# Kernel optimization log

Hardware: AMD Instinct MI355X
Metric: run time of the kernel (lower is better)

The kernel has to match this reference:

```python
import jax, jax.numpy as jnp
import numpy as np

B, T, C, H = 4, 2048, 1024, 16


def setup_inputs() -> dict:
    key = jax.random.key(0)
    k1, k2, k3 = jax.random.split(key, 3)
    x = jax.random.normal(k1, (B, T, C), dtype=jnp.float32)
    W_qkv = jax.random.normal(k2, (C, 3 * C), dtype=jnp.float32) * 0.02
    W_proj = jax.random.normal(k3, (C, C), dtype=jnp.float32) * 0.02
    return {"x": x, "W_qkv": W_qkv, "W_proj": W_proj}


def reference(x, W_qkv, W_proj):
    Bc, Tc, Cc = x.shape
    D = Cc // H
    qkv = x @ W_qkv                          # [B,T,3C]
    k, q, v = jnp.split(qkv, 3, axis=-1)     # split order k,q,v as in source
    q = q.reshape(Bc, Tc, H, D)
    k = k.reshape(Bc, Tc, H, D)
    v = v.reshape(Bc, Tc, H, D)
    # NOTE: module scales by full C**-0.5, not head_dim**-0.5
    scale = jnp.asarray(Cc, x.dtype) ** -0.5
    wei = jnp.einsum("bqhd,bkhd->bhqk", q, k) * scale      # [B,H,T,T]
    causal = jnp.tril(jnp.ones((Tc, Tc), dtype=bool))
    wei = jnp.where(causal[None, None], wei, jnp.asarray(-jnp.inf, x.dtype))
    att = jax.nn.softmax(wei, axis=-1)
    out = jnp.einsum("bhqk,bkhd->bqhd", att, v).reshape(Bc, Tc, Cc)
    return out @ W_proj
```

## Files before the change

kernel.cpp:

```cpp
#include <hip/hip_runtime.h>
#include <hip/hip_bf16.h>

#define B_   4
#define T_   2048
#define C_   1024
#define H_   16
#define D_   64
#define NQKV 3072
#define M_   (B_*T_)

typedef __attribute__((ext_vector_type(8))) short bf16x8;
typedef __attribute__((ext_vector_type(4))) short bf16x4;
typedef __attribute__((ext_vector_type(4))) float f32x4;
typedef __hip_bfloat16 bf16;

__device__ inline short f2bs(float f) {
    bf16 h = __float2bfloat16(f);
    return *(short*)&h;
}

__device__ inline void async_ld16(const bf16* g, const short* l) {
    __builtin_amdgcn_global_load_lds(
        (const __attribute__((address_space(1))) void*)g,
        (__attribute__((address_space(3))) void*)l, 16, 0, 0);
}

__global__ __launch_bounds__(256) void prep(const float* __restrict__ x,
                                            const float* __restrict__ Wqkv,
                                            const float* __restrict__ Wproj,
                                            bf16* __restrict__ xb,
                                            bf16* __restrict__ wqkv_t,
                                            bf16* __restrict__ wproj_t) {
    __shared__ short t[32][33];
    const int bid = blockIdx.x;
    if (bid < 4096) {
        const long i = ((long)bid * 256 + threadIdx.x) * 8;
        const float4 a = *(const float4*)(x + i);
        const float4 bq = *(const float4*)(x + i + 4);
        bf16x8 o;
        o[0] = f2bs(a.x); o[1] = f2bs(a.y); o[2] = f2bs(a.z); o[3] = f2bs(a.w);
        o[4] = f2bs(bq.x); o[5] = f2bs(bq.y); o[6] = f2bs(bq.z); o[7] = f2bs(bq.w);
        *(bf16x8*)(xb + i) = o;
        return;
    }
    const float* in;  bf16* out;  int R, Ccol, r0, c0;
    if (bid < 7168) {
        const int b2 = bid - 4096;
        in = Wqkv; out = wqkv_t; R = C_; Ccol = NQKV;
        c0 = (b2 % 96) * 32; r0 = (b2 / 96) * 32;
    } else {
        const int b3 = bid - 7168;
        in = Wproj; out = wproj_t; R = C_; Ccol = C_;
        c0 = (b3 % 32) * 32; r0 = (b3 / 32) * 32;
    }
    const int xx = threadIdx.x & 31, yy = threadIdx.x >> 5;
#pragma unroll
    for (int i = 0; i < 4; i++)
        t[yy + 8*i][xx] = f2bs(in[(long)(r0 + yy + 8*i) * Ccol + c0 + xx]);
    __syncthreads();
#pragma unroll
    for (int i = 0; i < 4; i++)
        ((short*)out)[(long)(c0 + yy + 8*i) * R + r0 + xx] = t[xx][yy + 8*i];
}

template<int MODE>
__global__ __launch_bounds__(256) void gemm_bt(const bf16* __restrict__ A,
                                               const bf16* __restrict__ Bt,
                                               float* __restrict__ outp,
                                               bf16* __restrict__ qb,
                                               bf16* __restrict__ kb,
                                               bf16* __restrict__ vbT,
                                               int K, int N) {
    __shared__ __align__(16) short SMEM[18432];
    short* As = SMEM;
    short* Bs = SMEM + 8192;
    const int tid  = threadIdx.x;
    const int w    = tid >> 6, lane = tid & 63;
    const int g    = lane >> 4, ln = lane & 15;
    const int m0   = blockIdx.y * 128, n0 = blockIdx.x * 128;
    const int wm   = w & 1, wn = w >> 1;

    f32x4 acc[4][4] = {};

    for (int k0 = 0; k0 < K; k0 += 64) {
#pragma unroll
        for (int i = 0; i < 4; i++) {
            const int s   = w * 256 + i * 64 + lane;
            const int row = s >> 3, c8 = (s & 7) ^ ((s >> 3) & 7);
            async_ld16(A  + (long)(m0 + row) * K + k0 + c8 * 8, &As[s * 8]);
            async_ld16(Bt + (long)(n0 + row) * K + k0 + c8 * 8, &Bs[s * 8]);
        }
        __syncthreads();

#pragma unroll
        for (int kh = 0; kh < 2; kh++) {
            bf16x8 af[4], bfr[4];
#pragma unroll
            for (int i = 0; i < 4; i++)
                af[i]  = *(const bf16x8*)&As[(wm * 64 + i * 16 + ln) * 64 + ((kh * 4 + g) ^ (ln & 7)) * 8];
#pragma unroll
            for (int j = 0; j < 4; j++)
                bfr[j] = *(const bf16x8*)&Bs[(wn * 64 + j * 16 + ln) * 64 + ((kh * 4 + g) ^ (ln & 7)) * 8];
#pragma unroll
            for (int i = 0; i < 4; i++)
#pragma unroll
                for (int j = 0; j < 4; j++)
                    acc[i][j] = __builtin_amdgcn_mfma_f32_16x16x32_bf16(af[i], bfr[j], acc[i][j], 0, 0, 0);
        }
        __syncthreads();
    }

    if (MODE == 0 && n0 >= 2048) {
        short* Vt = SMEM;
#pragma unroll
        for (int i = 0; i < 4; i++)
#pragma unroll
            for (int j = 0; j < 4; j++)
#pragma unroll
                for (int r = 0; r < 4; r++) {
                    const int tl = wm * 64 + i * 16 + g * 4 + r;
                    const int dl = wn * 64 + j * 16 + ln;
                    Vt[dl * 144 + tl] = f2bs(acc[i][j][r]);
                }
        __syncthreads();
        const int b  = m0 >> 11, tb = m0 & (T_ - 1);
        const int h0 = (n0 - 2048) >> 6;
#pragma unroll
        for (int ii = 0; ii < 8; ii++) {
            const int s = ii * 256 + tid;
            const int dl = s >> 4, t16 = s & 15;
            const bf16x8 v = *(const bf16x8*)&Vt[dl * 144 + t16 * 8];
            const int h = h0 + (dl >> 6), d = dl & 63;
            *(bf16x8*)&vbT[(((long)(b * H_ + h)) * D_ + d) * T_ + tb + t16 * 8] = v;
        }
        return;
    }

#pragma unroll
    for (int i = 0; i < 4; i++) {
#pragma unroll
        for (int j = 0; j < 4; j++) {
#pragma unroll
            for (int r = 0; r < 4; r++) {
                const int row = m0 + wm * 64 + i * 16 + g * 4 + r;
                const int col = n0 + wn * 64 + j * 16 + ln;
                if (MODE == 1) {
                    outp[(long)row * N + col] = acc[i][j][r];
                } else {
                    const int b = row >> 11, t = row & (T_ - 1);
                    const int seg = col >> 10;
                    const int c = col & (C_ - 1), h = c >> 6, d = c & 63;
                    if (seg == 0)
                        kb[(((long)(b * H_ + h)) * T_ + t) * D_ + d] = __float2bfloat16(acc[i][j][r]);
                    else
                        qb[(((long)(b * H_ + h)) * T_ + t) * D_ + d] = __float2bfloat16(acc[i][j][r] * 0.03125f);
                }
            }
        }
    }
}

__device__ inline void subtile(const bf16x8& qf0, const bf16x8& qf1,
                               f32x4* o, f32x4& l,
                               const short* Ks, const short* Vs, short* myP,
                               int q0, int kbase, int h2, int w, int g, int ln,
                               const bf16x8& ones) {
    f32x4 s[4] = {};
#pragma unroll
    for (int kj = 0; kj < 4; kj++) {
        const int krow = h2 * 64 + kj * 16 + ln;
        const bf16x8 kf0 = *(const bf16x8*)&Ks[krow * 64 + ((0 + g) ^ (krow & 7)) * 8];
        s[kj] = __builtin_amdgcn_mfma_f32_16x16x32_bf16(qf0, kf0, s[kj], 0, 0, 0);
        const bf16x8 kf1 = *(const bf16x8*)&Ks[krow * 64 + ((4 + g) ^ (krow & 7)) * 8];
        s[kj] = __builtin_amdgcn_mfma_f32_16x16x32_bf16(qf1, kf1, s[kj], 0, 0, 0);
    }
    const int rowg = q0 + w * 16 + g * 4;
    if (kbase == q0) {
#pragma unroll
        for (int kj = 0; kj < 4; kj++) {
            const int key = kbase + kj * 16 + ln;
#pragma unroll
            for (int r = 0; r < 4; r++) {
                float p = __expf(s[kj][r]);
                p = (key <= rowg + r) ? p : 0.f;
                const int prow = g * 4 + r;
                const int pc8 = (kj * 2 + (ln >> 3)) ^ (prow & 7);
                myP[prow * 64 + pc8 * 8 + (ln & 7)] = f2bs(p);
            }
        }
    } else {
#pragma unroll
        for (int kj = 0; kj < 4; kj++) {
#pragma unroll
            for (int r = 0; r < 4; r++) {
                const int prow = g * 4 + r;
                const int pc8 = (kj * 2 + (ln >> 3)) ^ (prow & 7);
                myP[prow * 64 + pc8 * 8 + (ln & 7)] = f2bs(__expf(s[kj][r]));
            }
        }
    }
    asm volatile("s_waitcnt lgkmcnt(0)" ::: "memory");
    const bf16x8 pf0 = *(const bf16x8*)&myP[ln * 64 + ((0 + g) ^ (ln & 7)) * 8];
    const bf16x8 pf1 = *(const bf16x8*)&myP[ln * 64 + ((4 + g) ^ (ln & 7)) * 8];
    l = __builtin_amdgcn_mfma_f32_16x16x32_bf16(ones, pf0, l, 0, 0, 0);
    l = __builtin_amdgcn_mfma_f32_16x16x32_bf16(ones, pf1, l, 0, 0, 0);
#pragma unroll
    for (int nb = 0; nb < 4; nb++) {
        const int drow = nb * 16 + ln;
        const bf16x8 vf0 = *(const bf16x8*)&Vs[drow * 128 + ((h2 * 8 + 0 + g) ^ (drow & 7)) * 8];
        o[nb] = __builtin_amdgcn_mfma_f32_16x16x32_bf16(vf0, pf0, o[nb], 0, 0, 0);
        const bf16x8 vf1 = *(const bf16x8*)&Vs[drow * 128 + ((h2 * 8 + 4 + g) ^ (drow & 7)) * 8];
        o[nb] = __builtin_amdgcn_mfma_f32_16x16x32_bf16(vf1, pf1, o[nb], 0, 0, 0);
    }
}

__global__ __launch_bounds__(256, 4) void flash(const bf16* __restrict__ qb,
                                                const bf16* __restrict__ kb,
                                                const bf16* __restrict__ vbT,
                                                bf16* __restrict__ att) {
    __shared__ __align__(16) short Ks[128 * 64];
    __shared__ __align__(16) short Vs[64 * 128];
    __shared__ __align__(16) short Ps[4 * 16 * 64];
    const int tid = threadIdx.x, w = tid >> 6, lane = tid & 63;
    const int g = lane >> 4, ln = lane & 15;
    const int lin = blockIdx.x;
    const int bh = lin & 63, p = lin >> 6;
    const int b = bh >> 4, h = bh & 15;
    const int q0A = p * 64, q0B = (31 - p) * 64;

    const bf16* qpA = qb + ((long)bh * T_ + q0A + w * 16 + ln) * D_;
    const bf16* qpB = qb + ((long)bh * T_ + q0B + w * 16 + ln) * D_;
    const bf16x8 qfA0 = *(const bf16x8*)(qpA + g * 8);
    const bf16x8 qfA1 = *(const bf16x8*)(qpA + 32 + g * 8);
    const bf16x8 qfB0 = *(const bf16x8*)(qpB + g * 8);
    const bf16x8 qfB1 = *(const bf16x8*)(qpB + 32 + g * 8);

    bf16x8 ones;
#pragma unroll
    for (int i = 0; i < 8; i++) ones[i] = 0x3F80;

    f32x4 oA[4] = {}, oB[4] = {};
    f32x4 lA = {}, lB = {};
    short* myP = &Ps[w * 16 * 64];

    const int nstB = (q0B + 64 + 127) >> 7;
    for (int s = 0; s < nstB; s++) {
        const int k0 = s * 128;
        bf16x8 kr[4], vr[4];
#pragma unroll
        for (int i = 0; i < 4; i++) {
            const int cc = i * 256 + tid;
            kr[i] = *(const bf16x8*)&kb [((long)bh * T_ + k0 + (cc >> 3)) * D_ + (cc & 7) * 8];
            vr[i] = *(const bf16x8*)&vbT[((long)bh * D_ + (cc >> 4)) * T_ + k0 + (cc & 15) * 8];
        }
        __syncthreads();
#pragma unroll
        for (int i = 0; i < 4; i++) {
            const int cc = i * 256 + tid;
            const int key = cc >> 3, c8 = cc & 7;
            *(bf16x8*)&Ks[key * 64 + (c8 ^ (key & 7)) * 8] = kr[i];
            const int d = cc >> 4, c16 = cc & 15;
            *(bf16x8*)&Vs[d * 128 + (c16 ^ (d & 7)) * 8] = vr[i];
        }
        __syncthreads();

#pragma unroll
        for (int h2 = 0; h2 < 2; h2++) {
            const int kbase = k0 + h2 * 64;
            if (kbase <= q0A + 63)
                subtile(qfA0, qfA1, oA, lA, Ks, Vs, myP, q0A, kbase, h2, w, g, ln, ones);
            if (kbase <= q0B + 63)
                subtile(qfB0, qfB1, oB, lB, Ks, Vs, myP, q0B, kbase, h2, w, g, ln, ones);
        }
    }

#pragma unroll
    for (int ti = 0; ti < 2; ti++) {
        const f32x4* o = ti ? oB : oA;
        const float invl = 1.f / (ti ? lB[0] : lA[0]);
        const int q = (ti ? q0B : q0A) + w * 16 + ln;
#pragma unroll
        for (int nb = 0; nb < 4; nb++) {
            bf16x4 pk;
#pragma unroll
            for (int r = 0; r < 4; r++) pk[r] = f2bs(o[nb][r] * invl);
            *(bf16x4*)&att[((long)b * T_ + q) * C_ + h * D_ + nb * 16 + g * 4] = pk;
        }
    }
}

extern "C" void kernel_launch(void* const* d_in, const int* in_sizes, int n_in,
                              void* d_out, int out_size, void* d_ws, size_t ws_size,
                              hipStream_t stream) {
    const float* x     = (const float*)d_in[0];
    const float* Wqkv  = (const float*)d_in[1];
    const float* Wproj = (const float*)d_in[2];
    float* out = (float*)d_out;

    char* ws = (char*)d_ws;
    bf16* wqkv_t  = (bf16*)(ws);
    bf16* wproj_t = (bf16*)(ws + 6291456);
    bf16* qb      = (bf16*)(ws + 8388608);
    bf16* kb      = (bf16*)(ws + 25165824);
    bf16* vbT     = (bf16*)(ws + 41943040);
    bf16* xb      = (bf16*)(ws + 58720256);
    bf16* att     = xb;
    (void)ws_size; (void)in_sizes; (void)n_in; (void)out_size;

    prep<<<dim3(8192), dim3(256), 0, stream>>>(x, Wqkv, Wproj, xb, wqkv_t, wproj_t);
    gemm_bt<0><<<dim3(NQKV / 128, M_ / 128), dim3(256), 0, stream>>>(
        xb, wqkv_t, (float*)nullptr, qb, kb, vbT, C_, NQKV);
    flash<<<dim3(1024), dim3(256), 0, stream>>>(qb, kb, vbT, att);
    gemm_bt<1><<<dim3(C_ / 128, M_ / 128), dim3(256), 0, stream>>>(
        att, wproj_t, out, (bf16*)nullptr, (bf16*)nullptr, (bf16*)nullptr, C_, C_);
}
```

Measured before the change: 251.3 us.

## Prefetch next K/V tile, fuse A/B subtiles, use exp2 and setprio

The global loads for the next 128-key K/V tile now go into registers right after the shared-memory barrier, so their latency overlaps the current tile's MFMA work instead of stalling at the top of each iteration. A new subtile_ab handles both query tiles (A and B) in one pass, sharing the K fragment reads and interleaving their score MFMAs. The log2(e) factor is folded into the Q pre-scale so the softmax can use the native exp2 instruction. s_setprio brackets raise wave priority around MFMA phases. The costs are more live registers from the prefetch buffers and the fused A/B state, which could reduce occupancy under launch_bounds(256,4).

After: 402.9 us. +60.4%, slower.

```diff
diff --git a/kernel.cpp b/kernel.cpp
--- a/kernel.cpp
+++ b/kernel.cpp
@@ -18,6 +18,8 @@
     bf16 h = __float2bfloat16(f);
     return *(short*)&h;
 }
+
+__device__ inline float exp2g(float f) { return __builtin_amdgcn_exp2f(f); }
 
 __device__ inline void async_ld16(const bf16* g, const short* l) {
     __builtin_amdgcn_global_load_lds(
@@ -153,12 +155,14 @@
                     if (seg == 0)
                         kb[(((long)(b * H_ + h)) * T_ + t) * D_ + d] = __float2bfloat16(acc[i][j][r]);
                     else
-                        qb[(((long)(b * H_ + h)) * T_ + t) * D_ + d] = __float2bfloat16(acc[i][j][r] * 0.03125f);
+                        qb[(((long)(b * H_ + h)) * T_ + t) * D_ + d] =
+                            __float2bfloat16(acc[i][j][r] * (0.03125f * 1.44269504f));
                 }
             }
         }
     }
 }
+
 
 __device__ inline void subtile(const bf16x8& qf0, const bf16x8& qf1,
                                f32x4* o, f32x4& l,
@@ -166,6 +170,7 @@
                                int q0, int kbase, int h2, int w, int g, int ln,
                                const bf16x8& ones) {
     f32x4 s[4] = {};
+    __builtin_amdgcn_s_setprio(1);
 #pragma unroll
     for (int kj = 0; kj < 4; kj++) {
         const int krow = h2 * 64 + kj * 16 + ln;
@@ -174,6 +179,7 @@
         const bf16x8 kf1 = *(const bf16x8*)&Ks[krow * 64 + ((4 + g) ^ (krow & 7)) * 8];
         s[kj] = __builtin_amdgcn_mfma_f32_16x16x32_bf16(qf1, kf1, s[kj], 0, 0, 0);
     }
+    __builtin_amdgcn_s_setprio(0);
     const int rowg = q0 + w * 16 + g * 4;
     if (kbase == q0) {
 #pragma unroll
@@ -181,7 +187,7 @@
             const int key = kbase + kj * 16 + ln;
 #pragma unroll
             for (int r = 0; r < 4; r++) {
-                float p = __expf(s[kj][r]);
+                float p = exp2g(s[kj][r]);
                 p = (key <= rowg + r) ? p : 0.f;
                 const int prow = g * 4 + r;
                 const int pc8 = (kj * 2 + (ln >> 3)) ^ (prow & 7);
@@ -195,7 +201,7 @@
             for (int r = 0; r < 4; r++) {
                 const int prow = g * 4 + r;
                 const int pc8 = (kj * 2 + (ln >> 3)) ^ (prow & 7);
-                myP[prow * 64 + pc8 * 8 + (ln & 7)] = f2bs(__expf(s[kj][r]));
+                myP[prow * 64 + pc8 * 8 + (ln & 7)] = f2bs(exp2g(s[kj][r]));
             }
         }
     }
@@ -204,6 +210,7 @@
     const bf16x8 pf1 = *(const bf16x8*)&myP[ln * 64 + ((4 + g) ^ (ln & 7)) * 8];
     l = __builtin_amdgcn_mfma_f32_16x16x32_bf16(ones, pf0, l, 0, 0, 0);
     l = __builtin_amdgcn_mfma_f32_16x16x32_bf16(ones, pf1, l, 0, 0, 0);
+    __builtin_amdgcn_s_setprio(1);
 #pragma unroll
     for (int nb = 0; nb < 4; nb++) {
         const int drow = nb * 16 + ln;
@@ -212,6 +219,90 @@
         const bf16x8 vf1 = *(const bf16x8*)&Vs[drow * 128 + ((h2 * 8 + 4 + g) ^ (drow & 7)) * 8];
         o[nb] = __builtin_amdgcn_mfma_f32_16x16x32_bf16(vf1, pf1, o[nb], 0, 0, 0);
     }
+    __builtin_amdgcn_s_setprio(0);
+}
+
+__device__ inline void subtile_ab(const bf16x8& qfA0, const bf16x8& qfA1,
+                                  const bf16x8& qfB0, const bf16x8& qfB1,
+                                  f32x4* oA, f32x4& lA, f32x4* oB, f32x4& lB,
+                                  const short* Ks, const short* Vs, short* myP,
+                                  int q0A, int kbase, int h2, int w, int g, int ln,
+                                  const bf16x8& ones, bool diagA) {
+    f32x4 sA[4] = {}, sB[4] = {};
+    __builtin_amdgcn_s_setprio(1);
+#pragma unroll
+    for (int kj = 0; kj < 4; kj++) {
+        const int krow = h2 * 64 + kj * 16 + ln;
+        const bf16x8 kf0 = *(const bf16x8*)&Ks[krow * 64 + ((0 + g) ^ (krow & 7)) * 8];
+        const bf16x8 kf1 = *(const bf16x8*)&Ks[krow * 64 + ((4 + g) ^ (krow & 7)) * 8];
+        sA[kj] = __builtin_amdgcn_mfma_f32_16x16x32_bf16(qfA0, kf0, sA[kj], 0, 0, 0);
+        sA[kj] = __builtin_amdgcn_mfma_f32_16x16x32_bf16(qfA1, kf1, sA[kj], 0, 0, 0);
+        sB[kj] = __builtin_amdgcn_mfma_f32_16x16x32_bf16(qfB0, kf0, sB[kj], 0, 0, 0);
+        sB[kj] = __builtin_amdgcn_mfma_f32_16x16x32_bf16(qfB1, kf1, sB[kj], 0, 0, 0);
+    }
+    __builtin_amdgcn_s_setprio(0);
+    const int rowg = q0A + w * 16 + g * 4;
+    if (diagA) {
+#pragma unroll
+        for (int kj = 0; kj < 4; kj++) {
+            const int key = kbase + kj * 16 + ln;
+#pragma unroll
+            for (int r = 0; r < 4; r++) {
+                float p = exp2g(sA[kj][r]);
+                p = (key <= rowg + r) ? p : 0.f;
+                const int prow = g * 4 + r;
+                const int pc8 = (kj * 2 + (ln >> 3)) ^ (prow & 7);
+                myP[prow * 64 + pc8 * 8 + (ln & 7)] = f2bs(p);
+            }
+        }
+    } else {
+#pragma unroll
+        for (int kj = 0; kj < 4; kj++)
+#pragma unroll
+            for (int r = 0; r < 4; r++) {
+                const int prow = g * 4 + r;
+                const int pc8 = (kj * 2 + (ln >> 3)) ^ (prow & 7);
+                myP[prow * 64 + pc8 * 8 + (ln & 7)] = f2bs(exp2g(sA[kj][r]));
+            }
+    }
+    asm volatile("s_waitcnt lgkmcnt(0)" ::: "memory");
+    const bf16x8 pfA0 = *(const bf16x8*)&myP[ln * 64 + ((0 + g) ^ (ln & 7)) * 8];
+    const bf16x8 pfA1 = *(const bf16x8*)&myP[ln * 64 + ((4 + g) ^ (ln & 7)) * 8];
+    lA = __builtin_amdgcn_mfma_f32_16x16x32_bf16(ones, pfA0, lA, 0, 0, 0);
+    lA = __builtin_amdgcn_mfma_f32_16x16x32_bf16(ones, pfA1, lA, 0, 0, 0);
+#pragma unroll
+    for (int kj = 0; kj < 4; kj++)
+#pragma unroll
+        for (int r = 0; r < 4; r++) {
+            const int prow = g * 4 + r;
+            const int pc8 = (kj * 2 + (ln >> 3)) ^ (prow & 7);
+            myP[prow * 64 + pc8 * 8 + (ln & 7)] = f2bs(exp2g(sB[kj][r]));
+        }
+    __builtin_amdgcn_s_setprio(1);
+#pragma unroll
+    for (int nb = 0; nb < 4; nb++) {
+        const int drow = nb * 16 + ln;
+        const bf16x8 vf0 = *(const bf16x8*)&Vs[drow * 128 + ((h2 * 8 + 0 + g) ^ (drow & 7)) * 8];
+        oA[nb] = __builtin_amdgcn_mfma_f32_16x16x32_bf16(vf0, pfA0, oA[nb], 0, 0, 0);
+        const bf16x8 vf1 = *(const bf16x8*)&Vs[drow * 128 + ((h2 * 8 + 4 + g) ^ (drow & 7)) * 8];
+        oA[nb] = __builtin_amdgcn_mfma_f32_16x16x32_bf16(vf1, pfA1, oA[nb], 0, 0, 0);
+    }
+    __builtin_amdgcn_s_setprio(0);
+    asm volatile("s_waitcnt lgkmcnt(0)" ::: "memory");
+    const bf16x8 pfB0 = *(const bf16x8*)&myP[ln * 64 + ((0 + g) ^ (ln & 7)) * 8];
+    const bf16x8 pfB1 = *(const bf16x8*)&myP[ln * 64 + ((4 + g) ^ (ln & 7)) * 8];
+    lB = __builtin_amdgcn_mfma_f32_16x16x32_bf16(ones, pfB0, lB, 0, 0, 0);
+    lB = __builtin_amdgcn_mfma_f32_16x16x32_bf16(ones, pfB1, lB, 0, 0, 0);
+    __builtin_amdgcn_s_setprio(1);
+#pragma unroll
+    for (int nb = 0; nb < 4; nb++) {
+        const int drow = nb * 16 + ln;
+        const bf16x8 vf0 = *(const bf16x8*)&Vs[drow * 128 + ((h2 * 8 + 0 + g) ^ (drow & 7)) * 8];
+        oB[nb] = __builtin_amdgcn_mfma_f32_16x16x32_bf16(vf0, pfB0, oB[nb], 0, 0, 0);
+        const bf16x8 vf1 = *(const bf16x8*)&Vs[drow * 128 + ((h2 * 8 + 4 + g) ^ (drow & 7)) * 8];
+        oB[nb] = __builtin_amdgcn_mfma_f32_16x16x32_bf16(vf1, pfB1, oB[nb], 0, 0, 0);
+    }
+    __builtin_amdgcn_s_setprio(0);
 }
 
 __global__ __launch_bounds__(256, 4) void flash(const bf16* __restrict__ qb,
@@ -244,15 +335,15 @@
     short* myP = &Ps[w * 16 * 64];
 
     const int nstB = (q0B + 64 + 127) >> 7;
+    bf16x8 kr[4], vr[4];
+#pragma unroll
+    for (int i = 0; i < 4; i++) {
+        const int cc = i * 256 + tid;
+        kr[i] = *(const bf16x8*)&kb [((long)bh * T_ + (cc >> 3)) * D_ + (cc & 7) * 8];
+        vr[i] = *(const bf16x8*)&vbT[((long)bh * D_ + (cc >> 4)) * T_ + (cc & 15) * 8];
+    }
     for (int s = 0; s < nstB; s++) {
         const int k0 = s * 128;
-        bf16x8 kr[4], vr[4];
-#pragma unroll
-        for (int i = 0; i < 4; i++) {
-            const int cc = i * 256 + tid;
-            kr[i] = *(const bf16x8*)&kb [((long)bh * T_ + k0 + (cc >> 3)) * D_ + (cc & 7) * 8];
-            vr[i] = *(const bf16x8*)&vbT[((long)bh * D_ + (cc >> 4)) * T_ + k0 + (cc & 15) * 8];
-        }
         __syncthreads();
 #pragma unroll
         for (int i = 0; i < 4; i++) {
@@ -263,13 +354,24 @@
             *(bf16x8*)&Vs[d * 128 + (c16 ^ (d & 7)) * 8] = vr[i];
         }
         __syncthreads();
+        if (s + 1 < nstB) {
+            const int kn = k0 + 128;
+#pragma unroll
+            for (int i = 0; i < 4; i++) {
+                const int cc = i * 256 + tid;
+                kr[i] = *(const bf16x8*)&kb [((long)bh * T_ + kn + (cc >> 3)) * D_ + (cc & 7) * 8];
+                vr[i] = *(const bf16x8*)&vbT[((long)bh * D_ + (cc >> 4)) * T_ + kn + (cc & 15) * 8];
+            }
+        }
 
 #pragma unroll
         for (int h2 = 0; h2 < 2; h2++) {
             const int kbase = k0 + h2 * 64;
             if (kbase <= q0A + 63)
-                subtile(qfA0, qfA1, oA, lA, Ks, Vs, myP, q0A, kbase, h2, w, g, ln, ones);
-            if (kbase <= q0B + 63)
+                subtile_ab(qfA0, qfA1, qfB0, qfB1, oA, lA, oB, lB,
+                           Ks, Vs, myP, q0A, kbase, h2, w, g, ln, ones,
+                           kbase == q0A);
+            else if (kbase <= q0B + 63)
                 subtile(qfB0, qfB1, oB, lB, Ks, Vs, myP, q0B, kbase, h2, w, g, ln, ones);
         }
     }
```
